# Kernel tuning notes

Hardware: AMD Instinct MI355X
Metric: run time of the kernel (lower is better)

Reference implementation:

```python
import jax, jax.numpy as jnp
import numpy as np

N_ORDER = 256
BATCH = 512
SEQ_LEN = 4096


def make_legs_matrices(N):
    # HiPPO-LegS: A[n,k] = -sqrt(2n+1)sqrt(2k+1) for n>k, -(n+1) for n==k, 0 for n<k
    # B[n] = sqrt(2n+1)
    q = np.arange(N, dtype=np.float64)
    r = np.sqrt(2.0 * q + 1.0)
    M = r[:, None] * r[None, :] * (q[:, None] > q[None, :]).astype(np.float64)
    M = M + np.diag(q + 1.0)
    A = -M
    B = r[:, None]
    return jnp.asarray(A, jnp.float32), jnp.asarray(B, jnp.float32)


def setup_inputs() -> dict:
    key = jax.random.key(0)
    A, Bm = make_legs_matrices(N_ORDER)
    f = jax.random.normal(key, (BATCH, SEQ_LEN), dtype=jnp.float32)
    init_state = jnp.zeros((BATCH, 1, N_ORDER), dtype=jnp.float32)
    return {"f": f, "A": A, "Bm": Bm, "init_state": init_state}


def reference(f, A, Bm, init_state):
    # Generalized bilinear transform discretization, alpha = 0.5, step = 1.0
    step = 1.0
    alpha = 0.5
    N = A.shape[0]
    I = jnp.eye(N, dtype=A.dtype)
    inv_step = 1.0 / step
    part1 = I - inv_step * alpha * A
    part2 = I + inv_step * (1.0 - alpha) * A
    # Original uses lstsq; part1 is nonsingular so solve is equivalent.
    Ad = jnp.linalg.solve(part1, part2)            # (N, N)
    Bd = jnp.linalg.solve(part1, inv_step * Bm)    # (N, 1)

    BdT = Bd.T[None]  # (1, 1, N)

    def step_fn(c, f_k):
        # c: (B, 1, N), f_k: (B,)
        # c_k = c_{k-1} @ Ad^T + Bd^T * f_k
        c = jnp.einsum('bin,mn->bim', c, Ad) + BdT * f_k[:, None, None]
        return c, None

    # scan over time axis; batch fully vectorized inside each step
    c_k, _ = jax.lax.scan(step_fn, init_state, jnp.swapaxes(f, 0, 1))
    return c_k  # (B, 1, N)
```

## Files before the change

### kernel.cpp

```cpp
#include <hip/hip_runtime.h>

#define NORD 256
#define TLEN 4096
#define HTLEN 2048
#define NBATCH 512


__device__ __forceinline__ void tile_fma4(const float (*As)[68], const float (*Bs)[68],
                                          int tr, int tc, float acc[4][4]) {
#pragma unroll
  for (int k = 0; k < 32; ++k) {
    const float4 a4 = *reinterpret_cast<const float4*>(&As[k][4 * tr]);
    const float4 b4 = *reinterpret_cast<const float4*>(&Bs[k][4 * tc]);
    const float a[4] = {a4.x, a4.y, a4.z, a4.w};
    const float b[4] = {b4.x, b4.y, b4.z, b4.w};
#pragma unroll
    for (int ii = 0; ii < 4; ++ii)
#pragma unroll
      for (int jj = 0; jj < 4; ++jj)
        acc[ii][jj] += a[ii] * b[jj];
  }
}

__device__ __forceinline__ void fill_tr(float (*dst)[68], const float* __restrict__ s0,
                                        const float* __restrict__ s1,
                                        int row0, int stride, int k0, int t) {
  const int rr = t >> 3, cc = (t & 7) << 2;
#pragma unroll
  for (int p = 0; p < 64; p += 32) {
    const size_t off = (size_t)(row0 + rr + p) * stride + k0 + cc;
    float4 v = *reinterpret_cast<const float4*>(s0 + off);
    if (s1) {
      const float4 w = *reinterpret_cast<const float4*>(s1 + off);
      v.x += w.x; v.y += w.y; v.z += w.z; v.w += w.w;
    }
    dst[cc + 0][rr + p] = v.x; dst[cc + 1][rr + p] = v.y;
    dst[cc + 2][rr + p] = v.z; dst[cc + 3][rr + p] = v.w;
  }
}

__global__ __launch_bounds__(256) void k_inv(const float* __restrict__ A,
                                             const float* __restrict__ Bm,
                                             float* __restrict__ P00, float* P01,
                                             float* __restrict__ U0, float* U1) {
  const int bid = blockIdx.x;
  const int i = threadIdx.x;
  const int wave = i >> 6, lane = i & 63;
  __shared__ float xs[NORD];
  float b = (bid < NORD) ? ((i == bid) ? 1.0f : 0.0f) : Bm[i];
  const float invd = 1.0f / (1.0f - 0.5f * A[i * NORD + i]);
  for (int w = 0; w < 4; ++w) {
    if (wave == w) {
      const int base = w << 6;
      for (int jj = 0; jj < 64; ++jj) {
        float bj = __shfl(b, jj);
        float dj = __shfl(invd, jj);
        float xj = bj * dj;
        if (lane > jj) {
          b += 0.5f * A[i * NORD + base + jj] * xj;
        } else if (lane == jj) {
          b = xj;
        }
      }
      xs[i] = b;
    }
    __syncthreads();
    if (wave > w) {
      const int base = w << 6;
      const float4* arow = reinterpret_cast<const float4*>(A + i * NORD + base);
#pragma unroll
      for (int q = 0; q < 16; ++q) {
        float4 a4 = arow[q];
        b += 0.5f * (a4.x * xs[base + 4 * q + 0] + a4.y * xs[base + 4 * q + 1] +
                     a4.z * xs[base + 4 * q + 2] + a4.w * xs[base + 4 * q + 3]);
      }
    }
  }
  if (bid < NORD) {
    P00[i * NORD + bid] = 2.0f * b - ((i == bid) ? 1.0f : 0.0f);
    if (P01) P01[(size_t)bid * 256 + i] = 0.0f;
  } else {
    U0[i] = b;
    if (U1) U1[i] = 0.0f;
  }
}

__global__ __launch_bounds__(256) void k_stage(float* U0, float* U1,
                                               const float* Pin0, const float* Pin1,
                                               float* Pout0, float* Pout1,
                                               int J, int n_apply) {
  const int bid = blockIdx.x;
  const int t = threadIdx.x;
  const int tr = t >> 4, tc = t & 15;
  __shared__ float As[32][68];
  __shared__ float Bs[32][68];
  const int kspan = U1 ? 128 : 256;

  if (bid < n_apply) {
    int work = bid, ks = 0;
    if (U1) { ks = work & 1; work >>= 1; }
    const int j0 = (work >> 2) << 6;
    const int m0 = (work & 3) << 6;
    const int klo = ks * kspan;
    float acc[4][4] = {};
    for (int kc = 0; kc < kspan; kc += 32) {
      const int k0 = klo + kc;
      fill_tr(As, U0, U1, j0, NORD, k0, t);
      fill_tr(Bs, Pin0, Pin1, m0, NORD, k0, t);
      __syncthreads();
      tile_fma4(As, Bs, tr, tc, acc);
      __syncthreads();
    }
    float* Ud = ks ? U1 : U0;
#pragma unroll
    for (int ii = 0; ii < 4; ++ii) {
      const int lr = j0 + 4 * tr + ii;
      if (lr < J) {
        float4 v = {acc[ii][0], acc[ii][1], acc[ii][2], acc[ii][3]};
        *reinterpret_cast<float4*>(&Ud[(size_t)(J + lr) * NORD + m0 + 4 * tc]) = v;
      }
    }
  } else {
    int q = bid - n_apply, ks = 0;
    if (Pin1) { ks = q & 1; q >>= 1; }
    const int m0s = (q >> 2) << 6;
    const int n0 = (q & 3) << 6;
    const int klo = ks * kspan;
    const int rr = t >> 3, cc = (t & 7) << 2;
    float acc[4][4] = {};
    for (int kc = 0; kc < kspan; kc += 32) {
      const int k0 = klo + kc;
      fill_tr(As, Pin0, Pin1, m0s, NORD, k0, t);
#pragma unroll
      for (int p = 0; p < 64; p += 32) {
        const size_t off = (size_t)(k0 + rr) * NORD + n0 + cc + p;
        float4 v = *reinterpret_cast<const float4*>(Pin0 + off);
        if (Pin1) {
          const float4 w = *reinterpret_cast<const float4*>(Pin1 + off);
          v.x += w.x; v.y += w.y; v.z += w.z; v.w += w.w;
        }
        *reinterpret_cast<float4*>(&Bs[rr][cc + p]) = v;
      }
      __syncthreads();
      tile_fma4(As, Bs, tr, tc, acc);
      __syncthreads();
    }
    float* Pd = ks ? Pout1 : Pout0;
#pragma unroll
    for (int ii = 0; ii < 4; ++ii) {
      float4 v = {acc[ii][0], acc[ii][1], acc[ii][2], acc[ii][3]};
      *reinterpret_cast<float4*>(&Pd[(size_t)(m0s + 4 * tr + ii) * NORD + n0 + 4 * tc]) = v;
    }
  }
}

__global__ __launch_bounds__(256) void k_final(const float* __restrict__ f,
                                               const float* __restrict__ U0,
                                               const float* U1,
                                               float* __restrict__ Glow,
                                               float* __restrict__ C) {
  const int bid = blockIdx.x;
  const int tile = bid & 31, ksf = bid >> 5;
  const int rt = tile >> 1, ct = tile & 1;
  const int h = rt >> 3;
  const int b0 = (rt & 7) << 6;
  const int m0 = ct << 7;
  const int jbase = ksf << 7;
  const int t = threadIdx.x;
  const int tr = t >> 4, tc = t & 15;
  __shared__ float As[32][68];
  __shared__ float Bs0[32][68];
  __shared__ float Bs1[32][68];
  const int rr = t >> 3, cc = (t & 7) << 2;
  const int jr = t >> 5, c32 = t & 31;
  float acc[4][8] = {};
  for (int kc = 0; kc < 128; kc += 32) {
    const int j0 = jbase + kc;
#pragma unroll
    for (int p = 0; p < 64; p += 32) {
      const float4 v = *reinterpret_cast<const float4*>(
          f + (size_t)(b0 + rr + p) * TLEN + HTLEN * h + j0 + cc);
      As[cc + 0][rr + p] = v.x; As[cc + 1][rr + p] = v.y;
      As[cc + 2][rr + p] = v.z; As[cc + 3][rr + p] = v.w;
    }
#pragma unroll
    for (int p = 0; p < 32; p += 8) {
      const int jj = jr + p;
      const size_t off = (size_t)(HTLEN - 1 - (j0 + jj)) * NORD + m0 + 4 * c32;
      float4 v = *reinterpret_cast<const float4*>(U0 + off);
      if (U1) {
        const float4 w = *reinterpret_cast<const float4*>(U1 + off);
        v.x += w.x; v.y += w.y; v.z += w.z; v.w += w.w;
      }
      if (c32 < 16) *reinterpret_cast<float4*>(&Bs0[jj][4 * c32]) = v;
      else          *reinterpret_cast<float4*>(&Bs1[jj][4 * (c32 - 16)]) = v;
    }
    __syncthreads();
#pragma unroll
    for (int k = 0; k < 32; ++k) {
      const float4 a4 = *reinterpret_cast<const float4*>(&As[k][4 * tr]);
      const float4 b4 = *reinterpret_cast<const float4*>(&Bs0[k][4 * tc]);
      const float4 b5 = *reinterpret_cast<const float4*>(&Bs1[k][4 * tc]);
      const float a[4] = {a4.x, a4.y, a4.z, a4.w};
      const float b[8] = {b4.x, b4.y, b4.z, b4.w, b5.x, b5.y, b5.z, b5.w};
#pragma unroll
      for (int ii = 0; ii < 4; ++ii)
#pragma unroll
        for (int jj = 0; jj < 8; ++jj)
          acc[ii][jj] += a[ii] * b[jj];
    }
    __syncthreads();
  }
  float* dst = h ? C : Glow;
#pragma unroll
  for (int ii = 0; ii < 4; ++ii) {
    const int row = b0 + 4 * tr + ii;
#pragma unroll
    for (int jj = 0; jj < 8; ++jj) {
      const int col = m0 + ((jj < 4) ? (4 * tc + jj) : (64 + 4 * tc + (jj - 4)));
      atomicAdd(dst + (size_t)row * NORD + col, acc[ii][jj]);
    }
  }
}

__global__ __launch_bounds__(256) void k_combine(const float* __restrict__ Glow,
                                                 const float* __restrict__ P0,
                                                 const float* P1,
                                                 float* __restrict__ C) {
  const int bid = blockIdx.x;
  const int b0 = (bid >> 2) << 6;
  const int m0 = (bid & 3) << 6;
  const int t = threadIdx.x;
  const int tr = t >> 4, tc = t & 15;
  __shared__ float As[32][68];
  __shared__ float Bs[32][68];
  float acc[4][4] = {};
  for (int k0 = 0; k0 < NORD; k0 += 32) {
    fill_tr(As, Glow, nullptr, b0, NORD, k0, t);
    fill_tr(Bs, P0, P1, m0, NORD, k0, t);
    __syncthreads();
    tile_fma4(As, Bs, tr, tc, acc);
    __syncthreads();
  }
#pragma unroll
  for (int ii = 0; ii < 4; ++ii)
#pragma unroll
    for (int jj = 0; jj < 4; ++jj) {
      float* p = C + (size_t)(b0 + 4 * tr + ii) * NORD + m0 + 4 * tc + jj;
      *p += acc[ii][jj];
    }
}

extern "C" void kernel_launch(void* const* d_in, const int* in_sizes, int n_in,
                              void* d_out, int out_size, void* d_ws, size_t ws_size,
                              hipStream_t stream) {
  const float* f  = (const float*)d_in[0];
  const float* A  = (const float*)d_in[1];
  const float* Bm = (const float*)d_in[2];

  float* ws = (float*)d_ws;
  const size_t need_split = (size_t)(4 * 65536 + 2 * 524288 + 131072) * sizeof(float);
  const int KS = (ws_size >= need_split) ? 2 : 1;

  float *P00, *P01, *P10, *P11, *U0, *U1, *Glow;
  if (KS == 2) {
    P00 = ws;            P01 = ws + 65536;
    P10 = ws + 131072;   P11 = ws + 196608;
    U0  = ws + 262144;   U1  = U0 + 524288;
    Glow = U0 + 1048576;
  } else {
    P00 = ws;            P01 = nullptr;
    P10 = ws + 65536;    P11 = nullptr;
    U0  = ws + 131072;   U1  = nullptr;
    Glow = ws + 655360;
  }
  float* C = (float*)d_out;

  hipMemsetAsync(d_out, 0, (size_t)NBATCH * NORD * sizeof(float), stream);
  hipMemsetAsync(Glow, 0, (size_t)NBATCH * NORD * sizeof(float), stream);

  hipLaunchKernelGGL(k_inv, dim3(NORD + 1), dim3(256), 0, stream, A, Bm, P00, P01, U0, U1);

  for (int s = 0; s <= 10; ++s) {
    const int J = 1 << s;
    const float* Pin0 = (s & 1) ? P10 : P00;
    const float* Pin1 = (s & 1) ? P11 : P01;
    float* Pout0 = (s & 1) ? P00 : P10;
    float* Pout1 = (s & 1) ? P01 : P11;
    const int rtiles = (J + 63) >> 6;
    const int n_apply = (rtiles << 2) * KS;
    const int n_sq = 16 * KS;
    hipLaunchKernelGGL(k_stage, dim3(n_apply + n_sq), dim3(256), 0, stream,
                       U0, U1, Pin0, Pin1, Pout0, Pout1, J, n_apply);
  }

  hipLaunchKernelGGL(k_final, dim3(512), dim3(256), 0, stream, f, U0, U1, Glow, C);
  hipLaunchKernelGGL(k_combine, dim3(32), dim3(256), 0, stream, Glow, P10, P11, C);
}
```

Before: 259.9 us.

## Drop split-K in doubling stages and replace atomics with partial-sum buffers

Removes the two-way K-split in the repeated-squaring stage kernels, so each matrix product runs with a single full-K pass over half as many blocks. The final contraction now writes 16 separate partial-sum slices with plain vector stores instead of atomicAdd, and the combine kernel adds up those slices. This also removes the two memsets. It trades atomic contention and memset launches for extra partial-buffer memory traffic, and gives the serial stage chain less parallelism per launch.

```diff
diff --git a/kernel.cpp b/kernel.cpp
--- a/kernel.cpp
+++ b/kernel.cpp
@@ -4,7 +4,6 @@
 #define TLEN 4096
 #define HTLEN 2048
 #define NBATCH 512
-
 
 __device__ __forceinline__ void tile_fma4(const float (*As)[68], const float (*Bs)[68],
                                           int tr, int tc, float acc[4][4]) {
@@ -23,17 +22,12 @@
 }
 
 __device__ __forceinline__ void fill_tr(float (*dst)[68], const float* __restrict__ s0,
-                                        const float* __restrict__ s1,
                                         int row0, int stride, int k0, int t) {
   const int rr = t >> 3, cc = (t & 7) << 2;
 #pragma unroll
   for (int p = 0; p < 64; p += 32) {
     const size_t off = (size_t)(row0 + rr + p) * stride + k0 + cc;
-    float4 v = *reinterpret_cast<const float4*>(s0 + off);
-    if (s1) {
-      const float4 w = *reinterpret_cast<const float4*>(s1 + off);
-      v.x += w.x; v.y += w.y; v.z += w.z; v.w += w.w;
-    }
+    const float4 v = *reinterpret_cast<const float4*>(s0 + off);
     dst[cc + 0][rr + p] = v.x; dst[cc + 1][rr + p] = v.y;
     dst[cc + 2][rr + p] = v.z; dst[cc + 3][rr + p] = v.w;
   }
@@ -41,8 +35,8 @@
 
 __global__ __launch_bounds__(256) void k_inv(const float* __restrict__ A,
                                              const float* __restrict__ Bm,
-                                             float* __restrict__ P00, float* P01,
-                                             float* __restrict__ U0, float* U1) {
+                                             float* __restrict__ Pa,
+                                             float* __restrict__ U) {
   const int bid = blockIdx.x;
   const int i = threadIdx.x;
   const int wave = i >> 6, lane = i & 63;
@@ -77,95 +71,77 @@
     }
   }
   if (bid < NORD) {
-    P00[i * NORD + bid] = 2.0f * b - ((i == bid) ? 1.0f : 0.0f);
-    if (P01) P01[(size_t)bid * 256 + i] = 0.0f;
+    Pa[i * NORD + bid] = 2.0f * b - ((i == bid) ? 1.0f : 0.0f);
   } else {
-    U0[i] = b;
-    if (U1) U1[i] = 0.0f;
-  }
-}
-
-__global__ __launch_bounds__(256) void k_stage(float* U0, float* U1,
-                                               const float* Pin0, const float* Pin1,
-                                               float* Pout0, float* Pout1,
+    U[i] = b;
+  }
+}
+
+__global__ __launch_bounds__(256) void k_stage(float* __restrict__ U,
+                                               const float* __restrict__ Pin,
+                                               float* __restrict__ Pout,
                                                int J, int n_apply) {
   const int bid = blockIdx.x;
   const int t = threadIdx.x;
   const int tr = t >> 4, tc = t & 15;
   __shared__ float As[32][68];
   __shared__ float Bs[32][68];
-  const int kspan = U1 ? 128 : 256;
 
   if (bid < n_apply) {
-    int work = bid, ks = 0;
-    if (U1) { ks = work & 1; work >>= 1; }
-    const int j0 = (work >> 2) << 6;
-    const int m0 = (work & 3) << 6;
-    const int klo = ks * kspan;
+    const int j0 = (bid >> 2) << 6;
+    const int m0 = (bid & 3) << 6;
     float acc[4][4] = {};
-    for (int kc = 0; kc < kspan; kc += 32) {
-      const int k0 = klo + kc;
-      fill_tr(As, U0, U1, j0, NORD, k0, t);
-      fill_tr(Bs, Pin0, Pin1, m0, NORD, k0, t);
+    for (int k0 = 0; k0 < NORD; k0 += 32) {
+      fill_tr(As, U, j0, NORD, k0, t);
+      fill_tr(Bs, Pin, m0, NORD, k0, t);
       __syncthreads();
       tile_fma4(As, Bs, tr, tc, acc);
       __syncthreads();
     }
-    float* Ud = ks ? U1 : U0;
 #pragma unroll
     for (int ii = 0; ii < 4; ++ii) {
       const int lr = j0 + 4 * tr + ii;
       if (lr < J) {
         float4 v = {acc[ii][0], acc[ii][1], acc[ii][2], acc[ii][3]};
-        *reinterpret_cast<float4*>(&Ud[(size_t)(J + lr) * NORD + m0 + 4 * tc]) = v;
+        *reinterpret_cast<float4*>(&U[(size_t)(J + lr) * NORD + m0 + 4 * tc]) = v;
       }
     }
   } else {
-    int q = bid - n_apply, ks = 0;
-    if (Pin1) { ks = q & 1; q >>= 1; }
+    const int q = bid - n_apply;
     const int m0s = (q >> 2) << 6;
     const int n0 = (q & 3) << 6;
-    const int klo = ks * kspan;
     const int rr = t >> 3, cc = (t & 7) << 2;
     float acc[4][4] = {};
-    for (int kc = 0; kc < kspan; kc += 32) {
-      const int k0 = klo + kc;
-      fill_tr(As, Pin0, Pin1, m0s, NORD, k0, t);
+    for (int k0 = 0; k0 < NORD; k0 += 32) {
+      fill_tr(As, Pin, m0s, NORD, k0, t);
 #pragma unroll
       for (int p = 0; p < 64; p += 32) {
         const size_t off = (size_t)(k0 + rr) * NORD + n0 + cc + p;
-        float4 v = *reinterpret_cast<const float4*>(Pin0 + off);
-        if (Pin1) {
-          const float4 w = *reinterpret_cast<const float4*>(Pin1 + off);
-          v.x += w.x; v.y += w.y; v.z += w.z; v.w += w.w;
-        }
-        *reinterpret_cast<float4*>(&Bs[rr][cc + p]) = v;
+        *reinterpret_cast<float4*>(&Bs[rr][cc + p]) =
+            *reinterpret_cast<const float4*>(Pin + off);
       }
       __syncthreads();
       tile_fma4(As, Bs, tr, tc, acc);
       __syncthreads();
     }
-    float* Pd = ks ? Pout1 : Pout0;
 #pragma unroll
     for (int ii = 0; ii < 4; ++ii) {
       float4 v = {acc[ii][0], acc[ii][1], acc[ii][2], acc[ii][3]};
-      *reinterpret_cast<float4*>(&Pd[(size_t)(m0s + 4 * tr + ii) * NORD + n0 + 4 * tc]) = v;
+      *reinterpret_cast<float4*>(&Pout[(size_t)(m0s + 4 * tr + ii) * NORD + n0 + 4 * tc]) = v;
     }
   }
 }
 
 __global__ __launch_bounds__(256) void k_final(const float* __restrict__ f,
-                                               const float* __restrict__ U0,
-                                               const float* U1,
-                                               float* __restrict__ Glow,
-                                               float* __restrict__ C) {
-  const int bid = blockIdx.x;
-  const int tile = bid & 31, ksf = bid >> 5;
-  const int rt = tile >> 1, ct = tile & 1;
-  const int h = rt >> 3;
-  const int b0 = (rt & 7) << 6;
+                                               const float* __restrict__ U,
+                                               float* __restrict__ Pp) {
+  const int bid = blockIdx.x;
+  const int split = bid & 7;
+  const int ct = (bid >> 3) & 1;
+  const int rt = (bid >> 4) & 7;
+  const int h = bid >> 7;
+  const int b0 = rt << 6;
   const int m0 = ct << 7;
-  const int jbase = ksf << 7;
   const int t = threadIdx.x;
   const int tr = t >> 4, tc = t & 15;
   __shared__ float As[32][68];
@@ -174,24 +150,20 @@
   const int rr = t >> 3, cc = (t & 7) << 2;
   const int jr = t >> 5, c32 = t & 31;
   float acc[4][8] = {};
-  for (int kc = 0; kc < 128; kc += 32) {
-    const int j0 = jbase + kc;
+  for (int ch = 0; ch < 8; ++ch) {
+    const int k0 = (split << 8) + (ch << 5);
 #pragma unroll
     for (int p = 0; p < 64; p += 32) {
       const float4 v = *reinterpret_cast<const float4*>(
-          f + (size_t)(b0 + rr + p) * TLEN + HTLEN * h + j0 + cc);
+          f + (size_t)(b0 + rr + p) * TLEN + HTLEN * h + k0 + cc);
       As[cc + 0][rr + p] = v.x; As[cc + 1][rr + p] = v.y;
       As[cc + 2][rr + p] = v.z; As[cc + 3][rr + p] = v.w;
     }
 #pragma unroll
     for (int p = 0; p < 32; p += 8) {
       const int jj = jr + p;
-      const size_t off = (size_t)(HTLEN - 1 - (j0 + jj)) * NORD + m0 + 4 * c32;
-      float4 v = *reinterpret_cast<const float4*>(U0 + off);
-      if (U1) {
-        const float4 w = *reinterpret_cast<const float4*>(U1 + off);
-        v.x += w.x; v.y += w.y; v.z += w.z; v.w += w.w;
-      }
+      const size_t off = (size_t)(HTLEN - 1 - (k0 + jj)) * NORD + m0 + 4 * c32;
+      const float4 v = *reinterpret_cast<const float4*>(U + off);
       if (c32 < 16) *reinterpret_cast<float4*>(&Bs0[jj][4 * c32]) = v;
       else          *reinterpret_cast<float4*>(&Bs1[jj][4 * (c32 - 16)]) = v;
     }
@@ -211,21 +183,19 @@
     }
     __syncthreads();
   }
-  float* dst = h ? C : Glow;
+  float* dst = Pp + (size_t)(h * 8 + split) * (NBATCH * NORD);
 #pragma unroll
   for (int ii = 0; ii < 4; ++ii) {
-    const int row = b0 + 4 * tr + ii;
-#pragma unroll
-    for (int jj = 0; jj < 8; ++jj) {
-      const int col = m0 + ((jj < 4) ? (4 * tc + jj) : (64 + 4 * tc + (jj - 4)));
-      atomicAdd(dst + (size_t)row * NORD + col, acc[ii][jj]);
-    }
-  }
-}
-
-__global__ __launch_bounds__(256) void k_combine(const float* __restrict__ Glow,
-                                                 const float* __restrict__ P0,
-                                                 const float* P1,
+    const size_t row = (size_t)(b0 + 4 * tr + ii) * NORD;
+    const float4 v0 = {acc[ii][0], acc[ii][1], acc[ii][2], acc[ii][3]};
+    const float4 v1 = {acc[ii][4], acc[ii][5], acc[ii][6], acc[ii][7]};
+    *reinterpret_cast<float4*>(&dst[row + m0 + 4 * tc]) = v0;
+    *reinterpret_cast<float4*>(&dst[row + m0 + 64 + 4 * tc]) = v1;
+  }
+}
+
+__global__ __launch_bounds__(256) void k_combine(const float* __restrict__ Pp,
+                                                 const float* __restrict__ Z,
                                                  float* __restrict__ C) {
   const int bid = blockIdx.x;
   const int b0 = (bid >> 2) << 6;
@@ -234,21 +204,39 @@
   const int tr = t >> 4, tc = t & 15;
   __shared__ float As[32][68];
   __shared__ float Bs[32][68];
+  const int rr = t >> 3, cc = (t & 7) << 2;
   float acc[4][4] = {};
   for (int k0 = 0; k0 < NORD; k0 += 32) {
-    fill_tr(As, Glow, nullptr, b0, NORD, k0, t);
-    fill_tr(Bs, P0, P1, m0, NORD, k0, t);
+#pragma unroll
+    for (int p = 0; p < 64; p += 32) {
+      const size_t off = (size_t)(b0 + rr + p) * NORD + k0 + cc;
+      float4 v = *reinterpret_cast<const float4*>(Pp + off);
+#pragma unroll
+      for (int sp = 1; sp < 8; ++sp) {
+        const float4 w = *reinterpret_cast<const float4*>(
+            Pp + (size_t)sp * (NBATCH * NORD) + off);
+        v.x += w.x; v.y += w.y; v.z += w.z; v.w += w.w;
+      }
+      As[cc + 0][rr + p] = v.x; As[cc + 1][rr + p] = v.y;
+      As[cc + 2][rr + p] = v.z; As[cc + 3][rr + p] = v.w;
+    }
+    fill_tr(Bs, Z, m0, NORD, k0, t);
     __syncthreads();
     tile_fma4(As, Bs, tr, tc, acc);
     __syncthreads();
   }
 #pragma unroll
-  for (int ii = 0; ii < 4; ++ii)
-#pragma unroll
-    for (int jj = 0; jj < 4; ++jj) {
-      float* p = C + (size_t)(b0 + 4 * tr + ii) * NORD + m0 + 4 * tc + jj;
-      *p += acc[ii][jj];
-    }
+  for (int ii = 0; ii < 4; ++ii) {
+    const size_t row = (size_t)(b0 + 4 * tr + ii) * NORD + m0 + 4 * tc;
+    float4 s = {acc[ii][0], acc[ii][1], acc[ii][2], acc[ii][3]};
+#pragma unroll
+    for (int sp = 8; sp < 16; ++sp) {
+      const float4 w = *reinterpret_cast<const float4*>(
+          Pp + (size_t)sp * (NBATCH * NORD) + row);
+      s.x += w.x; s.y += w.y; s.z += w.z; s.w += w.w;
+    }
+    *reinterpret_cast<float4*>(&C[row]) = s;
+  }
 }
 
 extern "C" void kernel_launch(void* const* d_in, const int* in_sizes, int n_in,
@@ -259,41 +247,24 @@
   const float* Bm = (const float*)d_in[2];
 
   float* ws = (float*)d_ws;
-  const size_t need_split = (size_t)(4 * 65536 + 2 * 524288 + 131072) * sizeof(float);
-  const int KS = (ws_size >= need_split) ? 2 : 1;
-
-  float *P00, *P01, *P10, *P11, *U0, *U1, *Glow;
-  if (KS == 2) {
-    P00 = ws;            P01 = ws + 65536;
-    P10 = ws + 131072;   P11 = ws + 196608;
-    U0  = ws + 262144;   U1  = U0 + 524288;
-    Glow = U0 + 1048576;
-  } else {
-    P00 = ws;            P01 = nullptr;
-    P10 = ws + 65536;    P11 = nullptr;
-    U0  = ws + 131072;   U1  = nullptr;
-    Glow = ws + 655360;
-  }
-  float* C = (float*)d_out;
-
-  hipMemsetAsync(d_out, 0, (size_t)NBATCH * NORD * sizeof(float), stream);
-  hipMemsetAsync(Glow, 0, (size_t)NBATCH * NORD * sizeof(float), stream);
-
-  hipLaunchKernelGGL(k_inv, dim3(NORD + 1), dim3(256), 0, stream, A, Bm, P00, P01, U0, U1);
+  float* Pa = ws;
+  float* Pb = ws + 65536;
+  float* U  = ws + 131072;
+  float* Pp = ws + 131072 + HTLEN * NORD;
+  float* C  = (float*)d_out;
+
+  hipLaunchKernelGGL(k_inv, dim3(NORD + 1), dim3(256), 0, stream, A, Bm, Pa, U);
 
   for (int s = 0; s <= 10; ++s) {
     const int J = 1 << s;
-    const float* Pin0 = (s & 1) ? P10 : P00;
-    const float* Pin1 = (s & 1) ? P11 : P01;
-    float* Pout0 = (s & 1) ? P00 : P10;
-    float* Pout1 = (s & 1) ? P01 : P11;
+    const float* Pin = (s & 1) ? Pb : Pa;
+    float* Pout = (s & 1) ? Pa : Pb;
     const int rtiles = (J + 63) >> 6;
-    const int n_apply = (rtiles << 2) * KS;
-    const int n_sq = 16 * KS;
-    hipLaunchKernelGGL(k_stage, dim3(n_apply + n_sq), dim3(256), 0, stream,
-                       U0, U1, Pin0, Pin1, Pout0, Pout1, J, n_apply);
-  }
-
-  hipLaunchKernelGGL(k_final, dim3(512), dim3(256), 0, stream, f, U0, U1, Glow, C);
-  hipLaunchKernelGGL(k_combine, dim3(32), dim3(256), 0, stream, Glow, P10, P11, C);
-}
+    const int n_apply = rtiles << 2;
+    hipLaunchKernelGGL(k_stage, dim3(n_apply + 16), dim3(256), 0, stream,
+                       U, Pin, Pout, J, n_apply);
+  }
+
+  hipLaunchKernelGGL(k_final, dim3(256), dim3(256), 0, stream, f, U, Pp);
+  hipLaunchKernelGGL(k_combine, dim3(32), dim3(256), 0, stream, Pp, Pb, C);
+}
```

Measured after the change: 253.6 us. 2.4% less time.
